# Optimization experiments

Measured on AMD Instinct MI355X. Metric: run time of the kernel, lower is better.

Reference implementation:

```python
import jax, jax.numpy as jnp
import numpy as np

PAIR = 128
HID = 64
EPS = 1e-5


def _ln(x, w, b):
    mu = jnp.mean(x, axis=-1, keepdims=True)
    var = jnp.mean((x - mu) ** 2, axis=-1, keepdims=True)
    return (x - mu) * jax.lax.rsqrt(var + EPS) * w + b


def setup_inputs() -> dict:
    key = jax.random.key(0)
    ks = jax.random.split(key, 8)
    B, N = 1, 448
    s_in = 1.0 / np.sqrt(PAIR)
    s_h = 1.0 / np.sqrt(HID)
    return {
        "z": jax.random.normal(ks[0], (B, N, N, PAIR), jnp.float32),
        "z_mask": jnp.ones((B, N, N), jnp.float32),
        "ln_w": jnp.ones((PAIR,), jnp.float32),
        "ln_b": jnp.zeros((PAIR,), jnp.float32),
        "lnh_w": jnp.ones((HID,), jnp.float32),
        "lnh_b": jnp.zeros((HID,), jnp.float32),
        "g1_w": jax.random.uniform(ks[1], (PAIR, HID), jnp.float32, -s_in, s_in),
        "g1_b": jnp.zeros((HID,), jnp.float32),
        "g2_w": jax.random.uniform(ks[2], (PAIR, HID), jnp.float32, -s_in, s_in),
        "g2_b": jnp.zeros((HID,), jnp.float32),
        "l1_w": jax.random.uniform(ks[3], (PAIR, HID), jnp.float32, -s_in, s_in),
        "l1_b": jnp.zeros((HID,), jnp.float32),
        "l2_w": jax.random.uniform(ks[4], (PAIR, HID), jnp.float32, -s_in, s_in),
        "l2_b": jnp.zeros((HID,), jnp.float32),
        "eg_w": jax.random.uniform(ks[5], (PAIR, PAIR), jnp.float32, -s_in, s_in),
        "eg_b": jnp.zeros((PAIR,), jnp.float32),
        "out_w": jax.random.uniform(ks[6], (HID, PAIR), jnp.float32, -s_h, s_h),
        "out_b": jnp.zeros((PAIR,), jnp.float32),
    }


def reference(z, z_mask, ln_w, ln_b, lnh_w, lnh_b, g1_w, g1_b, g2_w, g2_b,
              l1_w, l1_b, l2_w, l2_b, eg_w, eg_b, out_w, out_b):
    m = z_mask[..., None]                      # [B,N,N,1]
    zn = _ln(z, ln_w, ln_b)                    # [B,N,N,P]
    ab1 = jax.nn.sigmoid(zn @ g1_w + g1_b) * (zn @ l1_w + l1_b) * m  # [B,N,N,H]
    ab2 = jax.nn.sigmoid(zn @ g2_w + g2_b) * (zn @ l2_w + l2_b) * m  # [B,N,N,H]
    # outgoing + incoming triangle products, per channel c
    block = (jnp.einsum('bikc,bjkc->bijc', ab1, ab2)
             + jnp.einsum('bkic,bkjc->bijc', ab1, ab2))              # [B,N,N,H]
    out = jax.nn.sigmoid(zn @ eg_w + eg_b) * (_ln(block, lnh_w, lnh_b) @ out_w + out_b) * m
    return out
```

## Files before the change

kernel.cpp:

```cpp
#include <hip/hip_runtime.h>
#include <stdint.h>

#define N 448
#define NN (N*N)
#define P 128
#define H 64
#define PN 512
#define CH (PN*N)

typedef __attribute__((ext_vector_type(8))) short bf16x8;
typedef __attribute__((ext_vector_type(4))) float f32x4;
typedef __attribute__((ext_vector_type(16))) float f32x16;

__device__ __forceinline__ ushort f2bf(float f) {
    uint u = __builtin_bit_cast(uint, f);
    uint r = u + 0x7FFFu + ((u >> 16) & 1u);
    return (ushort)(r >> 16);
}
__device__ __forceinline__ float bf2f(ushort h) {
    uint u = ((uint)h) << 16;
    return __builtin_bit_cast(float, u);
}
__device__ __forceinline__ float sigmoidf(float x) {
    return 1.0f / (1.0f + __expf(-x));
}
__device__ __forceinline__ uint cvtpk(float lo, float hi) {
    uint r;
    asm("v_cvt_pk_bf16_f32 %0, %1, %2" : "=v"(r) : "v"(lo), "v"(hi));
    return r;
}

__global__ void k_prep(const float* __restrict__ g1w, const float* __restrict__ l1w,
                       const float* __restrict__ g2w, const float* __restrict__ l2w,
                       const float* __restrict__ egw,
                       ushort* __restrict__ wfrag) {
    int idx = blockIdx.x*256 + threadIdx.x;
    for (int e = idx; e < 24*4*64*8; e += gridDim.x*256) {
        int b  = e & 7;
        int l  = (e >> 3) & 63;
        int ks = (e >> 9) & 3;
        int ct = e >> 11;
        int k   = ks*32 + 8*(l>>4) + b;
        int col = ct*16 + (l & 15);
        float v;
        if (col < 64)       v = g1w[k*64 + col];
        else if (col < 128) v = l1w[k*64 + col - 64];
        else if (col < 192) v = g2w[k*64 + col - 128];
        else if (col < 256) v = l2w[k*64 + col - 192];
        else                v = egw[k*128 + col - 256];
        wfrag[e] = f2bf(v);
    }
}

__global__ __launch_bounds__(256) void k_proj(
    const float* __restrict__ z, const float* __restrict__ mask,
    const float* __restrict__ lnw, const float* __restrict__ lnb,
    const float* __restrict__ g1b, const float* __restrict__ l1b,
    const float* __restrict__ g2b, const float* __restrict__ l2b,
    const float* __restrict__ egb,
    const ushort* __restrict__ wfrag,
    ushort* __restrict__ abt, ushort* __restrict__ gsig)
{
    __shared__ ushort zn[64*128];
    const int t = threadIdx.x;
    const int w = t >> 6, l = t & 63;
    const int i = blockIdx.x / 7, j0 = (blockIdx.x % 7) * 64;

    {
        const int p = t >> 2;
        const int q = t & 3;
        const float* zp = z + (size_t)(i*N + j0 + p)*P + q*32;
        float4 v[8];
        #pragma unroll
        for (int x = 0; x < 8; ++x) v[x] = *(const float4*)(zp + x*4);
        float s = 0.f, sq = 0.f;
        #pragma unroll
        for (int x = 0; x < 8; ++x) {
            s  += v[x].x + v[x].y + v[x].z + v[x].w;
            sq += v[x].x*v[x].x + v[x].y*v[x].y + v[x].z*v[x].z + v[x].w*v[x].w;
        }
        s += __shfl_xor(s, 1);  sq += __shfl_xor(sq, 1);
        s += __shfl_xor(s, 2);  sq += __shfl_xor(sq, 2);
        float mu   = s * (1.0f/128.0f);
        float var  = sq * (1.0f/128.0f) - mu*mu;
        float rstd = rsqrtf(var + 1e-5f);
        #pragma unroll
        for (int cc = 0; cc < 4; ++cc) {
            int chunk = q*4 + cc;
            const float* lwp = lnw + chunk*8;
            const float* lbp = lnb + chunk*8;
            float4 lwa = *(const float4*)(lwp), lwb = *(const float4*)(lwp+4);
            float4 lba = *(const float4*)(lbp), lbb = *(const float4*)(lbp+4);
            float4 va = v[cc*2], vb = v[cc*2+1];
            float n0 = (va.x - mu)*rstd*lwa.x + lba.x;
            float n1 = (va.y - mu)*rstd*lwa.y + lba.y;
            float n2 = (va.z - mu)*rstd*lwa.z + lba.z;
            float n3 = (va.w - mu)*rstd*lwa.w + lba.w;
            float n4 = (vb.x - mu)*rstd*lwb.x + lbb.x;
            float n5 = (vb.y - mu)*rstd*lwb.y + lbb.y;
            float n6 = (vb.z - mu)*rstd*lwb.z + lbb.z;
            float n7 = (vb.w - mu)*rstd*lwb.w + lbb.w;
            uint4 pk;
            pk.x = cvtpk(n0, n1);
            pk.y = cvtpk(n2, n3);
            pk.z = cvtpk(n4, n5);
            pk.w = cvtpk(n6, n7);
            uint boff = (uint)p*256u + (((uint)(chunk ^ (p & 7)) & 15u) << 4);
            *(uint4*)((char*)zn + boff) = pk;
        }
    }
    __syncthreads();

    const int half = w & 1, pair = w >> 1;
    const uint lr = l & 15, lk = l >> 4;
    const float* mrow = mask + (size_t)i*N + j0;
    const float* gb = pair ? g2b : g1b;
    const float* lb = pair ? l2b : l1b;

    #pragma unroll 1
    for (int sub = 0; sub < 2; ++sub) {
        const int ctg = pair*8 + half*2 + sub;
        const int ctl = ctg + 4;
        f32x4 ag[4], al[4];
        #pragma unroll
        for (int mi = 0; mi < 4; ++mi) { ag[mi] = (f32x4){0,0,0,0}; al[mi] = (f32x4){0,0,0,0}; }

        #pragma unroll
        for (int ks = 0; ks < 4; ++ks) {
            bf16x8 bg  = *(const bf16x8*)(wfrag + ((size_t)(ctg*4 + ks)*64 + l)*8);
            bf16x8 blf = *(const bf16x8*)(wfrag + ((size_t)(ctl*4 + ks)*64 + l)*8);
            #pragma unroll
            for (int mi = 0; mi < 4; ++mi) {
                uint row = mi*16u + lr;
                uint chunk = (uint)(ks*4) + lk;
                bf16x8 af = *(const bf16x8*)((const char*)zn + row*256u + (((chunk ^ (row & 7u)) & 15u) << 4));
                ag[mi] = __builtin_amdgcn_mfma_f32_16x16x32_bf16(af, bg,  ag[mi], 0,0,0);
                al[mi] = __builtin_amdgcn_mfma_f32_16x16x32_bf16(af, blf, al[mi], 0,0,0);
            }
        }

        const int cidx = (half*2 + sub)*16 + (int)lr;
        const float gbias = gb[cidx];
        const float lbias = lb[cidx];
        #pragma unroll
        for (int mi = 0; mi < 4; ++mi) {
            float4 mv = *(const float4*)(mrow + mi*16 + (int)lk*4);
            float o0 = sigmoidf(ag[mi][0] + gbias) * (al[mi][0] + lbias) * mv.x;
            float o1 = sigmoidf(ag[mi][1] + gbias) * (al[mi][1] + lbias) * mv.y;
            float o2 = sigmoidf(ag[mi][2] + gbias) * (al[mi][2] + lbias) * mv.z;
            float o3 = sigmoidf(ag[mi][3] + gbias) * (al[mi][3] + lbias) * mv.w;
            uint2 pk;
            pk.x = cvtpk(o0, o1);
            pk.y = cvtpk(o2, o3);
            size_t off = (size_t)(pair*64 + cidx)*CH + (size_t)i*N + j0 + mi*16 + (int)lk*4;
            *(uint2*)(abt + off) = pk;
        }
    }

    {
        f32x4 ae[4][2];
        #pragma unroll
        for (int mi = 0; mi < 4; ++mi) { ae[mi][0] = (f32x4){0,0,0,0}; ae[mi][1] = (f32x4){0,0,0,0}; }

        #pragma unroll
        for (int ks = 0; ks < 4; ++ks) {
            bf16x8 b0 = *(const bf16x8*)(wfrag + ((size_t)((16 + w*2)*4 + ks)*64 + l)*8);
            bf16x8 b1 = *(const bf16x8*)(wfrag + ((size_t)((17 + w*2)*4 + ks)*64 + l)*8);
            #pragma unroll
            for (int mi = 0; mi < 4; ++mi) {
                uint row = mi*16u + lr;
                uint chunk = (uint)(ks*4) + lk;
                bf16x8 af = *(const bf16x8*)((const char*)zn + row*256u + (((chunk ^ (row & 7u)) & 15u) << 4));
                ae[mi][0] = __builtin_amdgcn_mfma_f32_16x16x32_bf16(af, b0, ae[mi][0], 0,0,0);
                ae[mi][1] = __builtin_amdgcn_mfma_f32_16x16x32_bf16(af, b1, ae[mi][1], 0,0,0);
            }
        }

        __syncthreads();

        float biasB[2];
        biasB[0] = egb[w*32 + (int)lr];
        biasB[1] = egb[w*32 + 16 + (int)lr];
        #pragma unroll
        for (int mi = 0; mi < 4; ++mi) {
            float4 mv = *(const float4*)(mrow + mi*16 + (int)lk*4);
            float mva[4] = { mv.x, mv.y, mv.z, mv.w };
            #pragma unroll
            for (int e = 0; e < 2; ++e) {
                uint cg = (uint)(w*32 + e*16) + lr;
                #pragma unroll
                for (int r = 0; r < 4; ++r) {
                    float sg = sigmoidf(ae[mi][e][r] + biasB[e]) * mva[r];
                    uint row = (uint)(mi*16) + lk*4u + (uint)r;
                    uint boff = row*256u + (((((cg >> 3) ^ (row & 7u)) & 15u)) << 4) + ((cg & 7u) << 1);
                    *(ushort*)((char*)zn + boff) = (ushort)cvtpk(sg, sg);
                }
            }
        }
    }
    __syncthreads();

    {
        int p2 = t >> 2, q2 = t & 3;
        size_t pos = (size_t)(i*N + j0 + p2);
        #pragma unroll
        for (int s2 = 0; s2 < 4; ++s2) {
            int chunk = q2*4 + s2;
            uint boff = (uint)p2*256u + (((uint)(chunk ^ (p2 & 7)) & 15u) << 4);
            uint4 vv = *(const uint4*)((const char*)zn + boff);
            *(uint4*)(gsig + pos*128 + q2*32 + s2*8) = vv;
        }
    }
}

__global__ __launch_bounds__(256) void k_transpose(const ushort* __restrict__ abt,
                                                   ushort* __restrict__ abtt) {
    int bid = blockIdx.x;
    int tile = bid % 49, a = bid / 49;
    int y0 = (tile / 7) * 64, x0 = (tile % 7) * 64;
    const ushort* src = abt  + (size_t)a*CH;
    ushort*       dst = abtt + (size_t)a*CH;
    __shared__ ushort tl[64][68];
    int t = threadIdx.x;
    #pragma unroll
    for (int q = 0; q < 4; ++q) {
        int f = q*1024 + t*4;
        int r = f >> 6, c4 = f & 63;
        ushort4 v = *(const ushort4*)(src + (size_t)(y0 + r)*N + x0 + c4);
        tl[r][c4] = v.x; tl[r][c4+1] = v.y; tl[r][c4+2] = v.z; tl[r][c4+3] = v.w;
    }
    __syncthreads();
    #pragma unroll
    for (int q = 0; q < 4; ++q) {
        int f = q*1024 + t*4;
        int r = f >> 6, c4 = f & 63;
        ushort4 v;
        v.x = tl[c4][r]; v.y = tl[c4+1][r]; v.z = tl[c4+2][r]; v.w = tl[c4+3][r];
        *(ushort4*)(dst + (size_t)(x0 + r)*N + y0 + c4) = v;
    }
}

__global__ __launch_bounds__(256) void k_tri(const ushort* __restrict__ abt,
                                             const ushort* __restrict__ abtt,
                                             float* __restrict__ blk) {
    int bid = (blockIdx.x & 7)*128 + (blockIdx.x >> 3);
    const int c = bid >> 4;
    const int tij = bid & 15;
    const int i0 = (tij >> 2) * 128, j0 = (tij & 3) * 128;
    const int t = threadIdx.x, w = t >> 6, l = t & 63;
    const int wr = w >> 1, wc = w & 1;
    const uint l31 = l & 31, kg = (uint)l >> 5;

    __shared__ ushort lds[4][128*64];

    const ushort* basep = (w >= 2) ? abtt : abt;
    const int chan = (w & 1) ? 64 + c : c;
    const int r0   = (w & 1) ? j0 : i0;
    const ushort* sbase = basep + (size_t)chan*CH + (size_t)r0*N;

    f32x16 acc[2][2];
    #pragma unroll
    for (int a = 0; a < 2; ++a)
        #pragma unroll
        for (int b = 0; b < 2; ++b) acc[a][b] = (f32x16){0,0,0,0,0,0,0,0,0,0,0,0,0,0,0,0};

    for (int kk = 0; kk < 7; ++kk) {
        __syncthreads();
        const ushort* sb = sbase + kk*64;
        #pragma unroll
        for (int q = 0; q < 16; ++q) {
            int r  = q*8 + (l >> 3);
            int ch = (l & 7) ^ (r & 7);
            const ushort* g = sb + (size_t)r*N + ch*8;
            __builtin_amdgcn_global_load_lds(
                (const __attribute__((address_space(1))) uint*)g,
                (__attribute__((address_space(3))) uint*)(&lds[w][q*512]),
                16, 0, 0);
        }
        __syncthreads();

        #pragma unroll
        for (int ks = 0; ks < 4; ++ks) {
            const uint chunk = (uint)(ks*2) + kg;
            {
                bf16x8 aA[2], bB[2];
                #pragma unroll
                for (int x = 0; x < 2; ++x) {
                    uint rowa = (uint)wr*64u + (uint)x*32u + l31;
                    uint rowb = (uint)wc*64u + (uint)x*32u + l31;
                    aA[x] = *(const bf16x8*)((const char*)lds[0] + rowa*128u + (((chunk ^ (rowa & 7u)) & 15u) << 4));
                    bB[x] = *(const bf16x8*)((const char*)lds[1] + rowb*128u + (((chunk ^ (rowb & 7u)) & 15u) << 4));
                }
                #pragma unroll
                for (int ra = 0; ra < 2; ++ra)
                    #pragma unroll
                    for (int cb = 0; cb < 2; ++cb)
                        acc[ra][cb] = __builtin_amdgcn_mfma_f32_32x32x16_bf16(aA[ra], bB[cb], acc[ra][cb], 0,0,0);
            }
            {
                bf16x8 aA[2], bB[2];
                #pragma unroll
                for (int x = 0; x < 2; ++x) {
                    uint rowa = (uint)wr*64u + (uint)x*32u + l31;
                    uint rowb = (uint)wc*64u + (uint)x*32u + l31;
                    aA[x] = *(const bf16x8*)((const char*)lds[2] + rowa*128u + (((chunk ^ (rowa & 7u)) & 15u) << 4));
                    bB[x] = *(const bf16x8*)((const char*)lds[3] + rowb*128u + (((chunk ^ (rowb & 7u)) & 15u) << 4));
                }
                #pragma unroll
                for (int ra = 0; ra < 2; ++ra)
                    #pragma unroll
                    for (int cb = 0; cb < 2; ++cb)
                        acc[ra][cb] = __builtin_amdgcn_mfma_f32_32x32x16_bf16(aA[ra], bB[cb], acc[ra][cb], 0,0,0);
            }
        }
    }

    #pragma unroll
    for (int ra = 0; ra < 2; ++ra) {
        #pragma unroll
        for (int cb = 0; cb < 2; ++cb) {
            int jb = j0 + wc*64 + cb*32 + (int)l31;
            if (jb < N) {
                #pragma unroll
                for (int r = 0; r < 16; ++r) {
                    int ii = i0 + wr*64 + ra*32 + (r & 3) + 8*(r >> 2) + 4*(int)kg;
                    if (ii < N) blk[(size_t)c*NN + (size_t)ii*N + jb] = acc[ra][cb][r];
                }
            }
        }
    }
}

__global__ __launch_bounds__(256) void k_out(const float* __restrict__ blk,
    const ushort* __restrict__ gsig,
    const float* __restrict__ lnhw, const float* __restrict__ lnhb,
    const float* __restrict__ outw, const float* __restrict__ outb,
    float* __restrict__ out)
{
    __shared__ float sblk[64][68];
    const int t = threadIdx.x;
    const int w = t >> 6, l = t & 63;
    const int pos0 = blockIdx.x * 64;

    #pragma unroll
    for (int q = 0; q < 4; ++q) {
        int flat = q*256 + t;
        int h = flat >> 4, f4 = flat & 15;
        float4 v = *(const float4*)(blk + (size_t)h*NN + pos0 + f4*4);
        sblk[f4*4+0][h] = v.x;
        sblk[f4*4+1][h] = v.y;
        sblk[f4*4+2][h] = v.z;
        sblk[f4*4+3][h] = v.w;
    }
    __syncthreads();

    {
        int p = w*16 + (l >> 2);
        int sub = l & 3;
        float vv[16];
        float s = 0.f, sq = 0.f;
        #pragma unroll
        for (int j = 0; j < 16; ++j) {
            float x = sblk[p][sub*16 + j];
            vv[j] = x; s += x; sq += x*x;
        }
        s += __shfl_xor(s, 1);  sq += __shfl_xor(sq, 1);
        s += __shfl_xor(s, 2);  sq += __shfl_xor(sq, 2);
        float mu   = s * (1.0f/64.0f);
        float var  = sq * (1.0f/64.0f) - mu*mu;
        float rstd = rsqrtf(var + 1e-5f);
        #pragma unroll
        for (int j = 0; j < 16; ++j) {
            float nv = (vv[j] - mu)*rstd*lnhw[sub*16+j] + lnhb[sub*16+j];
            sblk[p][sub*16 + j] = nv;
        }
    }
    __syncthreads();

    const int c4 = (t & 31) * 4;
    const int pg = t >> 5;
    float4 ob = *(const float4*)(outb + c4);

    #pragma unroll 1
    for (int hh = 0; hh < 2; ++hh) {
        const int prow = hh*32 + pg*4;
        float acc[4][4];
        #pragma unroll
        for (int j2 = 0; j2 < 4; ++j2)
            #pragma unroll
            for (int cc = 0; cc < 4; ++cc) acc[j2][cc] = 0.f;

        #pragma unroll 4
        for (int h4 = 0; h4 < 16; ++h4) {
            float4 wv[4];
            #pragma unroll
            for (int j = 0; j < 4; ++j)
                wv[j] = *(const float4*)(outw + (h4*4+j)*128 + c4);
            #pragma unroll
            for (int j2 = 0; j2 < 4; ++j2) {
                float4 av = *(const float4*)(&sblk[prow + j2][h4*4]);
                acc[j2][0] += av.x*wv[0].x + av.y*wv[1].x + av.z*wv[2].x + av.w*wv[3].x;
                acc[j2][1] += av.x*wv[0].y + av.y*wv[1].y + av.z*wv[2].y + av.w*wv[3].y;
                acc[j2][2] += av.x*wv[0].z + av.y*wv[1].z + av.z*wv[2].z + av.w*wv[3].z;
                acc[j2][3] += av.x*wv[0].w + av.y*wv[1].w + av.z*wv[2].w + av.w*wv[3].w;
            }
        }

        #pragma unroll
        for (int j2 = 0; j2 < 4; ++j2) {
            size_t pos = (size_t)(pos0 + prow + j2);
            ushort4 gv = *(const ushort4*)(gsig + pos*128 + c4);
            float4 res;
            res.x = bf2f(gv.x) * (acc[j2][0] + ob.x);
            res.y = bf2f(gv.y) * (acc[j2][1] + ob.y);
            res.z = bf2f(gv.z) * (acc[j2][2] + ob.z);
            res.w = bf2f(gv.w) * (acc[j2][3] + ob.w);
            *(float4*)(out + pos*128 + c4) = res;
        }
    }
}

extern "C" void kernel_launch(void* const* d_in, const int* in_sizes, int n_in,
                              void* d_out, int out_size, void* d_ws, size_t ws_size,
                              hipStream_t stream) {
    const float* z    = (const float*)d_in[0];
    const float* mask = (const float*)d_in[1];
    const float* lnw  = (const float*)d_in[2];
    const float* lnb  = (const float*)d_in[3];
    const float* lnhw = (const float*)d_in[4];
    const float* lnhb = (const float*)d_in[5];
    const float* g1w  = (const float*)d_in[6];
    const float* g1b  = (const float*)d_in[7];
    const float* g2w  = (const float*)d_in[8];
    const float* g2b  = (const float*)d_in[9];
    const float* l1w  = (const float*)d_in[10];
    const float* l1b  = (const float*)d_in[11];
    const float* l2w  = (const float*)d_in[12];
    const float* l2b  = (const float*)d_in[13];
    const float* egw  = (const float*)d_in[14];
    const float* egb  = (const float*)d_in[15];
    const float* outw = (const float*)d_in[16];
    const float* outb = (const float*)d_in[17];

    char* ws = (char*)d_ws;
    const size_t SZ_AB = (size_t)2*64*CH*2;
    const size_t SZ_G  = (size_t)NN*128*2;
    const size_t SZ_BL = (size_t)64*NN*4;
    ushort* abt    = (ushort*)ws;
    ushort* abtt   = (ushort*)(ws + SZ_AB);
    ushort* gsig   = (ushort*)(ws + 2*SZ_AB);
    float*  blkb   = (float*) (ws + 2*SZ_AB + SZ_G);
    ushort* wfrag  = (ushort*)(ws + 2*SZ_AB + SZ_G + SZ_BL);

    k_prep<<<32, 256, 0, stream>>>(g1w, l1w, g2w, l2w, egw, wfrag);
    k_proj<<<3136, 256, 0, stream>>>(z, mask, lnw, lnb, g1b, l1b, g2b, l2b, egb, wfrag, abt, gsig);
    k_transpose<<<128*49, 256, 0, stream>>>(abt, abtt);
    k_tri<<<64*16, 256, 0, stream>>>(abt, abtt, blkb);
    k_out<<<NN/64, 256, 0, stream>>>(blkb, gsig, lnhw, lnhb, outw, outb, (float*)d_out);
}
```

Baseline: 289.8 us.

## Split LayerNorm out of projection kernel and stage normalized z via direct LDS loads

The fused LayerNorm+projection kernel is split in two. A new kernel normalizes z and writes swizzled bf16 rows to a scratch buffer that reuses the block-output workspace. The matmul kernel then fills its LDS tile with global_load_lds direct-to-LDS copies. This is meant to shorten the matmul kernel's prologue and lower its register pressure, but it adds a launch and a bf16 round trip through global memory.

```diff
diff --git a/kernel.cpp b/kernel.cpp
--- a/kernel.cpp
+++ b/kernel.cpp
@@ -52,9 +52,57 @@
     }
 }
 
-__global__ __launch_bounds__(256) void k_proj(
-    const float* __restrict__ z, const float* __restrict__ mask,
+__global__ __launch_bounds__(256) void k_ln(
+    const float* __restrict__ z,
     const float* __restrict__ lnw, const float* __restrict__ lnb,
+    ushort* __restrict__ zng)
+{
+    const int t = threadIdx.x;
+    const int pos = blockIdx.x*64 + (t >> 2);
+    const int q = t & 3;
+    const float* zp = z + (size_t)pos*P + q*32;
+    float4 v[8];
+    #pragma unroll
+    for (int x = 0; x < 8; ++x) v[x] = *(const float4*)(zp + x*4);
+    float s = 0.f, sq = 0.f;
+    #pragma unroll
+    for (int x = 0; x < 8; ++x) {
+        s  += v[x].x + v[x].y + v[x].z + v[x].w;
+        sq += v[x].x*v[x].x + v[x].y*v[x].y + v[x].z*v[x].z + v[x].w*v[x].w;
+    }
+    s += __shfl_xor(s, 1);  sq += __shfl_xor(sq, 1);
+    s += __shfl_xor(s, 2);  sq += __shfl_xor(sq, 2);
+    float mu   = s * (1.0f/128.0f);
+    float var  = sq * (1.0f/128.0f) - mu*mu;
+    float rstd = rsqrtf(var + 1e-5f);
+    #pragma unroll
+    for (int cc = 0; cc < 4; ++cc) {
+        int chunk = q*4 + cc;
+        const float* lwp = lnw + chunk*8;
+        const float* lbp = lnb + chunk*8;
+        float4 lwa = *(const float4*)(lwp), lwb = *(const float4*)(lwp+4);
+        float4 lba = *(const float4*)(lbp), lbb = *(const float4*)(lbp+4);
+        float4 va = v[cc*2], vb = v[cc*2+1];
+        float n0 = (va.x - mu)*rstd*lwa.x + lba.x;
+        float n1 = (va.y - mu)*rstd*lwa.y + lba.y;
+        float n2 = (va.z - mu)*rstd*lwa.z + lba.z;
+        float n3 = (va.w - mu)*rstd*lwa.w + lba.w;
+        float n4 = (vb.x - mu)*rstd*lwb.x + lbb.x;
+        float n5 = (vb.y - mu)*rstd*lwb.y + lbb.y;
+        float n6 = (vb.z - mu)*rstd*lwb.z + lbb.z;
+        float n7 = (vb.w - mu)*rstd*lwb.w + lbb.w;
+        uint4 pk;
+        pk.x = cvtpk(n0, n1);
+        pk.y = cvtpk(n2, n3);
+        pk.z = cvtpk(n4, n5);
+        pk.w = cvtpk(n6, n7);
+        int slot = chunk ^ (pos & 7);
+        *(uint4*)(zng + (size_t)pos*128 + slot*8) = pk;
+    }
+}
+
+__global__ __launch_bounds__(256) void k_mm(
+    const ushort* __restrict__ zng, const float* __restrict__ mask,
     const float* __restrict__ g1b, const float* __restrict__ l1b,
     const float* __restrict__ g2b, const float* __restrict__ l2b,
     const float* __restrict__ egb,
@@ -67,46 +115,14 @@
     const int i = blockIdx.x / 7, j0 = (blockIdx.x % 7) * 64;
 
     {
-        const int p = t >> 2;
-        const int q = t & 3;
-        const float* zp = z + (size_t)(i*N + j0 + p)*P + q*32;
-        float4 v[8];
-        #pragma unroll
-        for (int x = 0; x < 8; ++x) v[x] = *(const float4*)(zp + x*4);
-        float s = 0.f, sq = 0.f;
-        #pragma unroll
-        for (int x = 0; x < 8; ++x) {
-            s  += v[x].x + v[x].y + v[x].z + v[x].w;
-            sq += v[x].x*v[x].x + v[x].y*v[x].y + v[x].z*v[x].z + v[x].w*v[x].w;
-        }
-        s += __shfl_xor(s, 1);  sq += __shfl_xor(sq, 1);
-        s += __shfl_xor(s, 2);  sq += __shfl_xor(sq, 2);
-        float mu   = s * (1.0f/128.0f);
-        float var  = sq * (1.0f/128.0f) - mu*mu;
-        float rstd = rsqrtf(var + 1e-5f);
-        #pragma unroll
-        for (int cc = 0; cc < 4; ++cc) {
-            int chunk = q*4 + cc;
-            const float* lwp = lnw + chunk*8;
-            const float* lbp = lnb + chunk*8;
-            float4 lwa = *(const float4*)(lwp), lwb = *(const float4*)(lwp+4);
-            float4 lba = *(const float4*)(lbp), lbb = *(const float4*)(lbp+4);
-            float4 va = v[cc*2], vb = v[cc*2+1];
-            float n0 = (va.x - mu)*rstd*lwa.x + lba.x;
-            float n1 = (va.y - mu)*rstd*lwa.y + lba.y;
-            float n2 = (va.z - mu)*rstd*lwa.z + lba.z;
-            float n3 = (va.w - mu)*rstd*lwa.w + lba.w;
-            float n4 = (vb.x - mu)*rstd*lwb.x + lbb.x;
-            float n5 = (vb.y - mu)*rstd*lwb.y + lbb.y;
-            float n6 = (vb.z - mu)*rstd*lwb.z + lbb.z;
-            float n7 = (vb.w - mu)*rstd*lwb.w + lbb.w;
-            uint4 pk;
-            pk.x = cvtpk(n0, n1);
-            pk.y = cvtpk(n2, n3);
-            pk.z = cvtpk(n4, n5);
-            pk.w = cvtpk(n6, n7);
-            uint boff = (uint)p*256u + (((uint)(chunk ^ (p & 7)) & 15u) << 4);
-            *(uint4*)((char*)zn + boff) = pk;
+        const ushort* src = zng + (size_t)(i*N + j0 + w*16)*128;
+        #pragma unroll
+        for (int qq = 0; qq < 4; ++qq) {
+            const ushort* g = src + (size_t)qq*512 + (l>>4)*128 + (l&15)*8;
+            __builtin_amdgcn_global_load_lds(
+                (const __attribute__((address_space(1))) uint*)g,
+                (__attribute__((address_space(3))) uint*)(&zn[(w*16 + qq*4)*128]),
+                16, 0, 0);
         }
     }
     __syncthreads();
@@ -451,9 +467,11 @@
     ushort* gsig   = (ushort*)(ws + 2*SZ_AB);
     float*  blkb   = (float*) (ws + 2*SZ_AB + SZ_G);
     ushort* wfrag  = (ushort*)(ws + 2*SZ_AB + SZ_G + SZ_BL);
+    ushort* zng    = (ushort*)blkb;
 
     k_prep<<<32, 256, 0, stream>>>(g1w, l1w, g2w, l2w, egw, wfrag);
-    k_proj<<<3136, 256, 0, stream>>>(z, mask, lnw, lnb, g1b, l1b, g2b, l2b, egb, wfrag, abt, gsig);
+    k_ln<<<3136, 256, 0, stream>>>(z, lnw, lnb, zng);
+    k_mm<<<3136, 256, 0, stream>>>(zng, mask, g1b, l1b, g2b, l2b, egb, wfrag, abt, gsig);
     k_transpose<<<128*49, 256, 0, stream>>>(abt, abtt);
     k_tri<<<64*16, 256, 0, stream>>>(abt, abtt, blkb);
     k_out<<<NN/64, 256, 0, stream>>>(blkb, gsig, lnhw, lnhb, outw, outb, (float*)d_out);
```

After: 307.0 us. 5.9% more time.

## Process two tiles per block in proj and out kernels with software pipelining

Applied to the files above, without the earlier changes.

k_proj now handles two i-rows per block. It prefetches the second row's z values into registers while the first row's matmuls run, and uses a double-buffered LDS with a separate gsig staging buffer. k_out handles four 64-position tiles per block, prefetching the next tile's block data into registers and alternating two LDS buffers. The aim is to hide global load latency behind compute. The cost is a quarter as many blocks in k_out, which lowers parallelism, plus more LDS and register use in both kernels, which may reduce occupancy.

```diff
diff --git a/kernel.cpp b/kernel.cpp
--- a/kernel.cpp
+++ b/kernel.cpp
@@ -52,71 +52,51 @@
     }
 }
 
-__global__ __launch_bounds__(256) void k_proj(
-    const float* __restrict__ z, const float* __restrict__ mask,
-    const float* __restrict__ lnw, const float* __restrict__ lnb,
-    const float* __restrict__ g1b, const float* __restrict__ l1b,
-    const float* __restrict__ g2b, const float* __restrict__ l2b,
-    const float* __restrict__ egb,
-    const ushort* __restrict__ wfrag,
-    ushort* __restrict__ abt, ushort* __restrict__ gsig)
-{
-    __shared__ ushort zn[64*128];
-    const int t = threadIdx.x;
-    const int w = t >> 6, l = t & 63;
-    const int i = blockIdx.x / 7, j0 = (blockIdx.x % 7) * 64;
-
-    {
-        const int p = t >> 2;
-        const int q = t & 3;
-        const float* zp = z + (size_t)(i*N + j0 + p)*P + q*32;
-        float4 v[8];
-        #pragma unroll
-        for (int x = 0; x < 8; ++x) v[x] = *(const float4*)(zp + x*4);
-        float s = 0.f, sq = 0.f;
-        #pragma unroll
-        for (int x = 0; x < 8; ++x) {
-            s  += v[x].x + v[x].y + v[x].z + v[x].w;
-            sq += v[x].x*v[x].x + v[x].y*v[x].y + v[x].z*v[x].z + v[x].w*v[x].w;
-        }
-        s += __shfl_xor(s, 1);  sq += __shfl_xor(sq, 1);
-        s += __shfl_xor(s, 2);  sq += __shfl_xor(sq, 2);
-        float mu   = s * (1.0f/128.0f);
-        float var  = sq * (1.0f/128.0f) - mu*mu;
-        float rstd = rsqrtf(var + 1e-5f);
-        #pragma unroll
-        for (int cc = 0; cc < 4; ++cc) {
-            int chunk = q*4 + cc;
-            const float* lwp = lnw + chunk*8;
-            const float* lbp = lnb + chunk*8;
-            float4 lwa = *(const float4*)(lwp), lwb = *(const float4*)(lwp+4);
-            float4 lba = *(const float4*)(lbp), lbb = *(const float4*)(lbp+4);
-            float4 va = v[cc*2], vb = v[cc*2+1];
-            float n0 = (va.x - mu)*rstd*lwa.x + lba.x;
-            float n1 = (va.y - mu)*rstd*lwa.y + lba.y;
-            float n2 = (va.z - mu)*rstd*lwa.z + lba.z;
-            float n3 = (va.w - mu)*rstd*lwa.w + lba.w;
-            float n4 = (vb.x - mu)*rstd*lwb.x + lbb.x;
-            float n5 = (vb.y - mu)*rstd*lwb.y + lbb.y;
-            float n6 = (vb.z - mu)*rstd*lwb.z + lbb.z;
-            float n7 = (vb.w - mu)*rstd*lwb.w + lbb.w;
-            uint4 pk;
-            pk.x = cvtpk(n0, n1);
-            pk.y = cvtpk(n2, n3);
-            pk.z = cvtpk(n4, n5);
-            pk.w = cvtpk(n6, n7);
-            uint boff = (uint)p*256u + (((uint)(chunk ^ (p & 7)) & 15u) << 4);
-            *(uint4*)((char*)zn + boff) = pk;
-        }
-    }
-    __syncthreads();
-
-    const int half = w & 1, pair = w >> 1;
+__device__ __forceinline__ void proj_ln(const float4* v, const float* __restrict__ lnw,
+                                        const float* __restrict__ lnb,
+                                        int p, int q, ushort* zn) {
+    float s = 0.f, sq = 0.f;
+    #pragma unroll
+    for (int x = 0; x < 8; ++x) {
+        s  += v[x].x + v[x].y + v[x].z + v[x].w;
+        sq += v[x].x*v[x].x + v[x].y*v[x].y + v[x].z*v[x].z + v[x].w*v[x].w;
+    }
+    s += __shfl_xor(s, 1);  sq += __shfl_xor(sq, 1);
+    s += __shfl_xor(s, 2);  sq += __shfl_xor(sq, 2);
+    float mu   = s * (1.0f/128.0f);
+    float var  = sq * (1.0f/128.0f) - mu*mu;
+    float rstd = rsqrtf(var + 1e-5f);
+    #pragma unroll
+    for (int cc = 0; cc < 4; ++cc) {
+        int chunk = q*4 + cc;
+        const float* lwp = lnw + chunk*8;
+        const float* lbp = lnb + chunk*8;
+        float4 lwa = *(const float4*)(lwp), lwb = *(const float4*)(lwp+4);
+        float4 lba = *(const float4*)(lbp), lbb = *(const float4*)(lbp+4);
+        float4 va = v[cc*2], vb = v[cc*2+1];
+        float n0 = (va.x - mu)*rstd*lwa.x + lba.x;
+        float n1 = (va.y - mu)*rstd*lwa.y + lba.y;
+        float n2 = (va.z - mu)*rstd*lwa.z + lba.z;
+        float n3 = (va.w - mu)*rstd*lwa.w + lba.w;
+        float n4 = (vb.x - mu)*rstd*lwb.x + lbb.x;
+        float n5 = (vb.y - mu)*rstd*lwb.y + lbb.y;
+        float n6 = (vb.z - mu)*rstd*lwb.z + lbb.z;
+        float n7 = (vb.w - mu)*rstd*lwb.w + lbb.w;
+        uint4 pk;
+        pk.x = cvtpk(n0, n1);
+        pk.y = cvtpk(n2, n3);
+        pk.z = cvtpk(n4, n5);
+        pk.w = cvtpk(n6, n7);
+        uint boff = (uint)p*256u + (((uint)(chunk ^ (p & 7)) & 15u) << 4);
+        *(uint4*)((char*)zn + boff) = pk;
+    }
+}
+
+__device__ __forceinline__ void proj_mm_ab(const ushort* zn, const ushort* __restrict__ wfrag,
+        const float* __restrict__ gb, const float* __restrict__ lb,
+        const float* __restrict__ mrow,
+        int i, int j0, int pair, int half, int l, ushort* __restrict__ abt) {
     const uint lr = l & 15, lk = l >> 4;
-    const float* mrow = mask + (size_t)i*N + j0;
-    const float* gb = pair ? g2b : g1b;
-    const float* lb = pair ? l2b : l1b;
-
     #pragma unroll 1
     for (int sub = 0; sub < 2; ++sub) {
         const int ctg = pair*8 + half*2 + sub;
@@ -124,7 +104,6 @@
         f32x4 ag[4], al[4];
         #pragma unroll
         for (int mi = 0; mi < 4; ++mi) { ag[mi] = (f32x4){0,0,0,0}; al[mi] = (f32x4){0,0,0,0}; }
-
         #pragma unroll
         for (int ks = 0; ks < 4; ++ks) {
             bf16x8 bg  = *(const bf16x8*)(wfrag + ((size_t)(ctg*4 + ks)*64 + l)*8);
@@ -138,7 +117,6 @@
                 al[mi] = __builtin_amdgcn_mfma_f32_16x16x32_bf16(af, blf, al[mi], 0,0,0);
             }
         }
-
         const int cidx = (half*2 + sub)*16 + (int)lr;
         const float gbias = gb[cidx];
         const float lbias = lb[cidx];
@@ -156,61 +134,113 @@
             *(uint2*)(abt + off) = pk;
         }
     }
-
+}
+
+__device__ __forceinline__ void proj_mm_eg(const ushort* zn, const ushort* __restrict__ wfrag,
+        const float* __restrict__ egb, const float* __restrict__ mrow,
+        int w, int l, ushort* gsbuf) {
+    const uint lr = l & 15, lk = l >> 4;
+    f32x4 ae[4][2];
+    #pragma unroll
+    for (int mi = 0; mi < 4; ++mi) { ae[mi][0] = (f32x4){0,0,0,0}; ae[mi][1] = (f32x4){0,0,0,0}; }
+    #pragma unroll
+    for (int ks = 0; ks < 4; ++ks) {
+        bf16x8 b0 = *(const bf16x8*)(wfrag + ((size_t)((16 + w*2)*4 + ks)*64 + l)*8);
+        bf16x8 b1 = *(const bf16x8*)(wfrag + ((size_t)((17 + w*2)*4 + ks)*64 + l)*8);
+        #pragma unroll
+        for (int mi = 0; mi < 4; ++mi) {
+            uint row = mi*16u + lr;
+            uint chunk = (uint)(ks*4) + lk;
+            bf16x8 af = *(const bf16x8*)((const char*)zn + row*256u + (((chunk ^ (row & 7u)) & 15u) << 4));
+            ae[mi][0] = __builtin_amdgcn_mfma_f32_16x16x32_bf16(af, b0, ae[mi][0], 0,0,0);
+            ae[mi][1] = __builtin_amdgcn_mfma_f32_16x16x32_bf16(af, b1, ae[mi][1], 0,0,0);
+        }
+    }
+    float biasB[2];
+    biasB[0] = egb[w*32 + (int)lr];
+    biasB[1] = egb[w*32 + 16 + (int)lr];
+    #pragma unroll
+    for (int mi = 0; mi < 4; ++mi) {
+        float4 mv = *(const float4*)(mrow + mi*16 + (int)lk*4);
+        float mva[4] = { mv.x, mv.y, mv.z, mv.w };
+        #pragma unroll
+        for (int e = 0; e < 2; ++e) {
+            uint cg = (uint)(w*32 + e*16) + lr;
+            #pragma unroll
+            for (int r = 0; r < 4; ++r) {
+                float sg = sigmoidf(ae[mi][e][r] + biasB[e]) * mva[r];
+                uint row = (uint)(mi*16) + lk*4u + (uint)r;
+                uint boff = row*256u + (((((cg >> 3) ^ (row & 7u)) & 15u)) << 4) + ((cg & 7u) << 1);
+                *(ushort*)((char*)gsbuf + boff) = (ushort)cvtpk(sg, sg);
+            }
+        }
+    }
+}
+
+__device__ __forceinline__ void proj_gsig_store(const ushort* gsbuf, ushort* __restrict__ gsig,
+        int i, int j0, int t) {
+    int p2 = t >> 2, q2 = t & 3;
+    size_t pos = (size_t)(i*N + j0 + p2);
+    #pragma unroll
+    for (int s2 = 0; s2 < 4; ++s2) {
+        int chunk = q2*4 + s2;
+        uint boff = (uint)p2*256u + (((uint)(chunk ^ (p2 & 7)) & 15u) << 4);
+        uint4 vv = *(const uint4*)((const char*)gsbuf + boff);
+        *(uint4*)(gsig + pos*128 + q2*32 + s2*8) = vv;
+    }
+}
+
+__global__ __launch_bounds__(256) void k_proj(
+    const float* __restrict__ z, const float* __restrict__ mask,
+    const float* __restrict__ lnw, const float* __restrict__ lnb,
+    const float* __restrict__ g1b, const float* __restrict__ l1b,
+    const float* __restrict__ g2b, const float* __restrict__ l2b,
+    const float* __restrict__ egb,
+    const ushort* __restrict__ wfrag,
+    ushort* __restrict__ abt, ushort* __restrict__ gsig)
+{
+    __shared__ ushort zn2[2][64*128];
+    __shared__ ushort gsbuf[64*128];
+    const int t = threadIdx.x;
+    const int w = t >> 6, l = t & 63;
+    const int ia = (blockIdx.x / 7) * 2, ib = ia + 1;
+    const int j0 = (blockIdx.x % 7) * 64;
+    const int p = t >> 2, q = t & 3;
+    const int half = w & 1, pair = w >> 1;
+    const float* mrowA = mask + (size_t)ia*N + j0;
+    const float* mrowB = mask + (size_t)ib*N + j0;
+    const float* gb = pair ? g2b : g1b;
+    const float* lb = pair ? l2b : l1b;
+
+    float4 vA[8];
     {
-        f32x4 ae[4][2];
-        #pragma unroll
-        for (int mi = 0; mi < 4; ++mi) { ae[mi][0] = (f32x4){0,0,0,0}; ae[mi][1] = (f32x4){0,0,0,0}; }
-
-        #pragma unroll
-        for (int ks = 0; ks < 4; ++ks) {
-            bf16x8 b0 = *(const bf16x8*)(wfrag + ((size_t)((16 + w*2)*4 + ks)*64 + l)*8);
-            bf16x8 b1 = *(const bf16x8*)(wfrag + ((size_t)((17 + w*2)*4 + ks)*64 + l)*8);
-            #pragma unroll
-            for (int mi = 0; mi < 4; ++mi) {
-                uint row = mi*16u + lr;
-                uint chunk = (uint)(ks*4) + lk;
-                bf16x8 af = *(const bf16x8*)((const char*)zn + row*256u + (((chunk ^ (row & 7u)) & 15u) << 4));
-                ae[mi][0] = __builtin_amdgcn_mfma_f32_16x16x32_bf16(af, b0, ae[mi][0], 0,0,0);
-                ae[mi][1] = __builtin_amdgcn_mfma_f32_16x16x32_bf16(af, b1, ae[mi][1], 0,0,0);
-            }
-        }
-
-        __syncthreads();
-
-        float biasB[2];
-        biasB[0] = egb[w*32 + (int)lr];
-        biasB[1] = egb[w*32 + 16 + (int)lr];
-        #pragma unroll
-        for (int mi = 0; mi < 4; ++mi) {
-            float4 mv = *(const float4*)(mrow + mi*16 + (int)lk*4);
-            float mva[4] = { mv.x, mv.y, mv.z, mv.w };
-            #pragma unroll
-            for (int e = 0; e < 2; ++e) {
-                uint cg = (uint)(w*32 + e*16) + lr;
-                #pragma unroll
-                for (int r = 0; r < 4; ++r) {
-                    float sg = sigmoidf(ae[mi][e][r] + biasB[e]) * mva[r];
-                    uint row = (uint)(mi*16) + lk*4u + (uint)r;
-                    uint boff = row*256u + (((((cg >> 3) ^ (row & 7u)) & 15u)) << 4) + ((cg & 7u) << 1);
-                    *(ushort*)((char*)zn + boff) = (ushort)cvtpk(sg, sg);
-                }
-            }
-        }
+        const float* zp = z + (size_t)(ia*N + j0 + p)*P + q*32;
+        #pragma unroll
+        for (int x = 0; x < 8; ++x) vA[x] = *(const float4*)(zp + x*4);
+    }
+    proj_ln(vA, lnw, lnb, p, q, zn2[0]);
+
+    float4 vB[8];
+    {
+        const float* zp = z + (size_t)(ib*N + j0 + p)*P + q*32;
+        #pragma unroll
+        for (int x = 0; x < 8; ++x) vB[x] = *(const float4*)(zp + x*4);
     }
     __syncthreads();
 
-    {
-        int p2 = t >> 2, q2 = t & 3;
-        size_t pos = (size_t)(i*N + j0 + p2);
-        #pragma unroll
-        for (int s2 = 0; s2 < 4; ++s2) {
-            int chunk = q2*4 + s2;
-            uint boff = (uint)p2*256u + (((uint)(chunk ^ (p2 & 7)) & 15u) << 4);
-            uint4 vv = *(const uint4*)((const char*)zn + boff);
-            *(uint4*)(gsig + pos*128 + q2*32 + s2*8) = vv;
-        }
-    }
+    proj_mm_ab(zn2[0], wfrag, gb, lb, mrowA, ia, j0, pair, half, l, abt);
+    proj_mm_eg(zn2[0], wfrag, egb, mrowA, w, l, gsbuf);
+    proj_ln(vB, lnw, lnb, p, q, zn2[1]);
+    __syncthreads();
+
+    proj_gsig_store(gsbuf, gsig, ia, j0, t);
+    proj_mm_ab(zn2[1], wfrag, gb, lb, mrowB, ib, j0, pair, half, l, abt);
+    __syncthreads();
+
+    proj_mm_eg(zn2[1], wfrag, egb, mrowB, w, l, gsbuf);
+    __syncthreads();
+
+    proj_gsig_store(gsbuf, gsig, ib, j0, t);
 }
 
 __global__ __launch_bounds__(256) void k_transpose(const ushort* __restrict__ abt,
@@ -337,85 +367,106 @@
     const float* __restrict__ outw, const float* __restrict__ outb,
     float* __restrict__ out)
 {
-    __shared__ float sblk[64][68];
+    __shared__ float sblk[2][64][68];
     const int t = threadIdx.x;
     const int w = t >> 6, l = t & 63;
-    const int pos0 = blockIdx.x * 64;
-
-    #pragma unroll
-    for (int q = 0; q < 4; ++q) {
-        int flat = q*256 + t;
+    const int base = blockIdx.x * 256;
+
+    float4 pre[4];
+    #pragma unroll
+    for (int qq = 0; qq < 4; ++qq) {
+        int flat = qq*256 + t;
         int h = flat >> 4, f4 = flat & 15;
-        float4 v = *(const float4*)(blk + (size_t)h*NN + pos0 + f4*4);
-        sblk[f4*4+0][h] = v.x;
-        sblk[f4*4+1][h] = v.y;
-        sblk[f4*4+2][h] = v.z;
-        sblk[f4*4+3][h] = v.w;
-    }
-    __syncthreads();
-
-    {
-        int p = w*16 + (l >> 2);
-        int sub = l & 3;
-        float vv[16];
-        float s = 0.f, sq = 0.f;
-        #pragma unroll
-        for (int j = 0; j < 16; ++j) {
-            float x = sblk[p][sub*16 + j];
-            vv[j] = x; s += x; sq += x*x;
-        }
-        s += __shfl_xor(s, 1);  sq += __shfl_xor(sq, 1);
-        s += __shfl_xor(s, 2);  sq += __shfl_xor(sq, 2);
-        float mu   = s * (1.0f/64.0f);
-        float var  = sq * (1.0f/64.0f) - mu*mu;
-        float rstd = rsqrtf(var + 1e-5f);
-        #pragma unroll
-        for (int j = 0; j < 16; ++j) {
-            float nv = (vv[j] - mu)*rstd*lnhw[sub*16+j] + lnhb[sub*16+j];
-            sblk[p][sub*16 + j] = nv;
-        }
-    }
-    __syncthreads();
-
-    const int c4 = (t & 31) * 4;
-    const int pg = t >> 5;
-    float4 ob = *(const float4*)(outb + c4);
+        pre[qq] = *(const float4*)(blk + (size_t)h*NN + base + f4*4);
+    }
 
     #pragma unroll 1
-    for (int hh = 0; hh < 2; ++hh) {
-        const int prow = hh*32 + pg*4;
-        float acc[4][4];
-        #pragma unroll
-        for (int j2 = 0; j2 < 4; ++j2)
-            #pragma unroll
-            for (int cc = 0; cc < 4; ++cc) acc[j2][cc] = 0.f;
-
-        #pragma unroll 4
-        for (int h4 = 0; h4 < 16; ++h4) {
-            float4 wv[4];
-            #pragma unroll
-            for (int j = 0; j < 4; ++j)
-                wv[j] = *(const float4*)(outw + (h4*4+j)*128 + c4);
+    for (int tt = 0; tt < 4; ++tt) {
+        const int b = tt & 1;
+        const int pos0 = base + tt*64;
+
+        #pragma unroll
+        for (int qq = 0; qq < 4; ++qq) {
+            int flat = qq*256 + t;
+            int h = flat >> 4, f4 = flat & 15;
+            sblk[b][f4*4+0][h] = pre[qq].x;
+            sblk[b][f4*4+1][h] = pre[qq].y;
+            sblk[b][f4*4+2][h] = pre[qq].z;
+            sblk[b][f4*4+3][h] = pre[qq].w;
+        }
+        if (tt < 3) {
+            #pragma unroll
+            for (int qq = 0; qq < 4; ++qq) {
+                int flat = qq*256 + t;
+                int h = flat >> 4, f4 = flat & 15;
+                pre[qq] = *(const float4*)(blk + (size_t)h*NN + pos0 + 64 + f4*4);
+            }
+        }
+        __syncthreads();
+
+        {
+            int p = w*16 + (l >> 2);
+            int sub = l & 3;
+            float vv[16];
+            float s = 0.f, sq = 0.f;
+            #pragma unroll
+            for (int j = 0; j < 16; ++j) {
+                float x = sblk[b][p][sub*16 + j];
+                vv[j] = x; s += x; sq += x*x;
+            }
+            s += __shfl_xor(s, 1);  sq += __shfl_xor(sq, 1);
+            s += __shfl_xor(s, 2);  sq += __shfl_xor(sq, 2);
+            float mu   = s * (1.0f/64.0f);
+            float var  = sq * (1.0f/64.0f) - mu*mu;
+            float rstd = rsqrtf(var + 1e-5f);
+            #pragma unroll
+            for (int j = 0; j < 16; ++j) {
+                float nv = (vv[j] - mu)*rstd*lnhw[sub*16+j] + lnhb[sub*16+j];
+                sblk[b][p][sub*16 + j] = nv;
+            }
+        }
+        __syncthreads();
+
+        const int c4 = (t & 31) * 4;
+        const int pg = t >> 5;
+        float4 ob = *(const float4*)(outb + c4);
+
+        #pragma unroll 1
+        for (int hh = 0; hh < 2; ++hh) {
+            const int prow = hh*32 + pg*4;
+            float acc[4][4];
+            #pragma unroll
+            for (int j2 = 0; j2 < 4; ++j2)
+                #pragma unroll
+                for (int cc = 0; cc < 4; ++cc) acc[j2][cc] = 0.f;
+
+            #pragma unroll 4
+            for (int h4 = 0; h4 < 16; ++h4) {
+                float4 wv[4];
+                #pragma unroll
+                for (int j = 0; j < 4; ++j)
+                    wv[j] = *(const float4*)(outw + (h4*4+j)*128 + c4);
+                #pragma unroll
+                for (int j2 = 0; j2 < 4; ++j2) {
+                    float4 av = *(const float4*)(&sblk[b][prow + j2][h4*4]);
+                    acc[j2][0] += av.x*wv[0].x + av.y*wv[1].x + av.z*wv[2].x + av.w*wv[3].x;
+                    acc[j2][1] += av.x*wv[0].y + av.y*wv[1].y + av.z*wv[2].y + av.w*wv[3].y;
+                    acc[j2][2] += av.x*wv[0].z + av.y*wv[1].z + av.z*wv[2].z + av.w*wv[3].z;
+                    acc[j2][3] += av.x*wv[0].w + av.y*wv[1].w + av.z*wv[2].w + av.w*wv[3].w;
+                }
+            }
+
             #pragma unroll
             for (int j2 = 0; j2 < 4; ++j2) {
-                float4 av = *(const float4*)(&sblk[prow + j2][h4*4]);
-                acc[j2][0] += av.x*wv[0].x + av.y*wv[1].x + av.z*wv[2].x + av.w*wv[3].x;
-                acc[j2][1] += av.x*wv[0].y + av.y*wv[1].y + av.z*wv[2].y + av.w*wv[3].y;
-                acc[j2][2] += av.x*wv[0].z + av.y*wv[1].z + av.z*wv[2].z + av.w*wv[3].z;
-                acc[j2][3] += av.x*wv[0].w + av.y*wv[1].w + av.z*wv[2].w + av.w*wv[3].w;
-            }
-        }
-
-        #pragma unroll
-        for (int j2 = 0; j2 < 4; ++j2) {
-            size_t pos = (size_t)(pos0 + prow + j2);
-            ushort4 gv = *(const ushort4*)(gsig + pos*128 + c4);
-            float4 res;
-            res.x = bf2f(gv.x) * (acc[j2][0] + ob.x);
-            res.y = bf2f(gv.y) * (acc[j2][1] + ob.y);
-            res.z = bf2f(gv.z) * (acc[j2][2] + ob.z);
-            res.w = bf2f(gv.w) * (acc[j2][3] + ob.w);
-            *(float4*)(out + pos*128 + c4) = res;
+                size_t pos = (size_t)(pos0 + prow + j2);
+                ushort4 gv = *(const ushort4*)(gsig + pos*128 + c4);
+                float4 res;
+                res.x = bf2f(gv.x) * (acc[j2][0] + ob.x);
+                res.y = bf2f(gv.y) * (acc[j2][1] + ob.y);
+                res.z = bf2f(gv.z) * (acc[j2][2] + ob.z);
+                res.w = bf2f(gv.w) * (acc[j2][3] + ob.w);
+                *(float4*)(out + pos*128 + c4) = res;
+            }
         }
     }
 }
@@ -453,8 +504,8 @@
     ushort* wfrag  = (ushort*)(ws + 2*SZ_AB + SZ_G + SZ_BL);
 
     k_prep<<<32, 256, 0, stream>>>(g1w, l1w, g2w, l2w, egw, wfrag);
-    k_proj<<<3136, 256, 0, stream>>>(z, mask, lnw, lnb, g1b, l1b, g2b, l2b, egb, wfrag, abt, gsig);
+    k_proj<<<1568, 256, 0, stream>>>(z, mask, lnw, lnb, g1b, l1b, g2b, l2b, egb, wfrag, abt, gsig);
     k_transpose<<<128*49, 256, 0, stream>>>(abt, abtt);
     k_tri<<<64*16, 256, 0, stream>>>(abt, abtt, blkb);
-    k_out<<<NN/64, 256, 0, stream>>>(blkb, gsig, lnhw, lnhb, outw, outb, (float*)d_out);
-}
+    k_out<<<NN/256, 256, 0, stream>>>(blkb, gsig, lnhw, lnhb, outw, outb, (float*)d_out);
+}
```

Measured after the change: 296.2 us. +2.2%, slower.

## Stage projection stores through LDS and prefetch blk tiles in output kernel

Applied to the files above, without the earlier changes.

In k_proj, the gated projection outputs are first written to a shared-memory staging tile and then copied to global memory as 16-byte coalesced rows, replacing scattered 8-byte stores. The mask loads are hoisted out of the loops and reused. k_out now processes four 64-position tiles per block, using a double-buffered LDS tile and prefetching the next tile's blk data into registers while the current one is normalised and projected. This adds shared memory per block, which may lower occupancy, and launches a quarter as many blocks for k_out.

```diff
diff --git a/kernel.cpp b/kernel.cpp
--- a/kernel.cpp
+++ b/kernel.cpp
@@ -62,6 +62,7 @@
     ushort* __restrict__ abt, ushort* __restrict__ gsig)
 {
     __shared__ ushort zn[64*128];
+    __shared__ ushort abstage[128*72];
     const int t = threadIdx.x;
     const int w = t >> 6, l = t & 63;
     const int i = blockIdx.x / 7, j0 = (blockIdx.x % 7) * 64;
@@ -117,6 +118,10 @@
     const float* gb = pair ? g2b : g1b;
     const float* lb = pair ? l2b : l1b;
 
+    float4 mv4[4];
+    #pragma unroll
+    for (int mi = 0; mi < 4; ++mi) mv4[mi] = *(const float4*)(mrow + mi*16 + (int)lk*4);
+
     #pragma unroll 1
     for (int sub = 0; sub < 2; ++sub) {
         const int ctg = pair*8 + half*2 + sub;
@@ -142,9 +147,10 @@
         const int cidx = (half*2 + sub)*16 + (int)lr;
         const float gbias = gb[cidx];
         const float lbias = lb[cidx];
+        const int srow = pair*64 + cidx;
         #pragma unroll
         for (int mi = 0; mi < 4; ++mi) {
-            float4 mv = *(const float4*)(mrow + mi*16 + (int)lk*4);
+            float4 mv = mv4[mi];
             float o0 = sigmoidf(ag[mi][0] + gbias) * (al[mi][0] + lbias) * mv.x;
             float o1 = sigmoidf(ag[mi][1] + gbias) * (al[mi][1] + lbias) * mv.y;
             float o2 = sigmoidf(ag[mi][2] + gbias) * (al[mi][2] + lbias) * mv.z;
@@ -152,8 +158,19 @@
             uint2 pk;
             pk.x = cvtpk(o0, o1);
             pk.y = cvtpk(o2, o3);
-            size_t off = (size_t)(pair*64 + cidx)*CH + (size_t)i*N + j0 + mi*16 + (int)lk*4;
-            *(uint2*)(abt + off) = pk;
+            *(uint2*)(abstage + (size_t)srow*72 + mi*16 + (int)lk*4) = pk;
+        }
+    }
+    __syncthreads();
+
+    {
+        int r = t >> 1, hh2 = t & 1;
+        const ushort* sp = abstage + (size_t)r*72 + hh2*32;
+        ushort* dp = abt + (size_t)r*CH + (size_t)i*N + j0 + hh2*32;
+        #pragma unroll
+        for (int k2 = 0; k2 < 4; ++k2) {
+            uint4 vv = *(const uint4*)(sp + k2*8);
+            *(uint4*)(dp + k2*8) = vv;
         }
     }
 
@@ -183,7 +200,7 @@
         biasB[1] = egb[w*32 + 16 + (int)lr];
         #pragma unroll
         for (int mi = 0; mi < 4; ++mi) {
-            float4 mv = *(const float4*)(mrow + mi*16 + (int)lk*4);
+            float4 mv = mv4[mi];
             float mva[4] = { mv.x, mv.y, mv.z, mv.w };
             #pragma unroll
             for (int e = 0; e < 2; ++e) {
@@ -337,85 +354,106 @@
     const float* __restrict__ outw, const float* __restrict__ outb,
     float* __restrict__ out)
 {
-    __shared__ float sblk[64][68];
+    __shared__ float sblk[2][64][68];
     const int t = threadIdx.x;
     const int w = t >> 6, l = t & 63;
-    const int pos0 = blockIdx.x * 64;
-
-    #pragma unroll
-    for (int q = 0; q < 4; ++q) {
-        int flat = q*256 + t;
+    const int base = blockIdx.x * 256;
+
+    float4 pre[4];
+    #pragma unroll
+    for (int qq = 0; qq < 4; ++qq) {
+        int flat = qq*256 + t;
         int h = flat >> 4, f4 = flat & 15;
-        float4 v = *(const float4*)(blk + (size_t)h*NN + pos0 + f4*4);
-        sblk[f4*4+0][h] = v.x;
-        sblk[f4*4+1][h] = v.y;
-        sblk[f4*4+2][h] = v.z;
-        sblk[f4*4+3][h] = v.w;
-    }
-    __syncthreads();
-
-    {
-        int p = w*16 + (l >> 2);
-        int sub = l & 3;
-        float vv[16];
-        float s = 0.f, sq = 0.f;
-        #pragma unroll
-        for (int j = 0; j < 16; ++j) {
-            float x = sblk[p][sub*16 + j];
-            vv[j] = x; s += x; sq += x*x;
-        }
-        s += __shfl_xor(s, 1);  sq += __shfl_xor(sq, 1);
-        s += __shfl_xor(s, 2);  sq += __shfl_xor(sq, 2);
-        float mu   = s * (1.0f/64.0f);
-        float var  = sq * (1.0f/64.0f) - mu*mu;
-        float rstd = rsqrtf(var + 1e-5f);
-        #pragma unroll
-        for (int j = 0; j < 16; ++j) {
-            float nv = (vv[j] - mu)*rstd*lnhw[sub*16+j] + lnhb[sub*16+j];
-            sblk[p][sub*16 + j] = nv;
-        }
-    }
-    __syncthreads();
-
-    const int c4 = (t & 31) * 4;
-    const int pg = t >> 5;
-    float4 ob = *(const float4*)(outb + c4);
+        pre[qq] = *(const float4*)(blk + (size_t)h*NN + base + f4*4);
+    }
 
     #pragma unroll 1
-    for (int hh = 0; hh < 2; ++hh) {
-        const int prow = hh*32 + pg*4;
-        float acc[4][4];
-        #pragma unroll
-        for (int j2 = 0; j2 < 4; ++j2)
-            #pragma unroll
-            for (int cc = 0; cc < 4; ++cc) acc[j2][cc] = 0.f;
-
-        #pragma unroll 4
-        for (int h4 = 0; h4 < 16; ++h4) {
-            float4 wv[4];
-            #pragma unroll
-            for (int j = 0; j < 4; ++j)
-                wv[j] = *(const float4*)(outw + (h4*4+j)*128 + c4);
+    for (int tt = 0; tt < 4; ++tt) {
+        const int b = tt & 1;
+        const int pos0 = base + tt*64;
+
+        #pragma unroll
+        for (int qq = 0; qq < 4; ++qq) {
+            int flat = qq*256 + t;
+            int h = flat >> 4, f4 = flat & 15;
+            sblk[b][f4*4+0][h] = pre[qq].x;
+            sblk[b][f4*4+1][h] = pre[qq].y;
+            sblk[b][f4*4+2][h] = pre[qq].z;
+            sblk[b][f4*4+3][h] = pre[qq].w;
+        }
+        if (tt < 3) {
+            #pragma unroll
+            for (int qq = 0; qq < 4; ++qq) {
+                int flat = qq*256 + t;
+                int h = flat >> 4, f4 = flat & 15;
+                pre[qq] = *(const float4*)(blk + (size_t)h*NN + pos0 + 64 + f4*4);
+            }
+        }
+        __syncthreads();
+
+        {
+            int p = w*16 + (l >> 2);
+            int sub = l & 3;
+            float vv[16];
+            float s = 0.f, sq = 0.f;
+            #pragma unroll
+            for (int j = 0; j < 16; ++j) {
+                float x = sblk[b][p][sub*16 + j];
+                vv[j] = x; s += x; sq += x*x;
+            }
+            s += __shfl_xor(s, 1);  sq += __shfl_xor(sq, 1);
+            s += __shfl_xor(s, 2);  sq += __shfl_xor(sq, 2);
+            float mu   = s * (1.0f/64.0f);
+            float var  = sq * (1.0f/64.0f) - mu*mu;
+            float rstd = rsqrtf(var + 1e-5f);
+            #pragma unroll
+            for (int j = 0; j < 16; ++j) {
+                float nv = (vv[j] - mu)*rstd*lnhw[sub*16+j] + lnhb[sub*16+j];
+                sblk[b][p][sub*16 + j] = nv;
+            }
+        }
+        __syncthreads();
+
+        const int c4 = (t & 31) * 4;
+        const int pg = t >> 5;
+        float4 ob = *(const float4*)(outb + c4);
+
+        #pragma unroll 1
+        for (int hh = 0; hh < 2; ++hh) {
+            const int prow = hh*32 + pg*4;
+            float acc[4][4];
+            #pragma unroll
+            for (int j2 = 0; j2 < 4; ++j2)
+                #pragma unroll
+                for (int cc = 0; cc < 4; ++cc) acc[j2][cc] = 0.f;
+
+            #pragma unroll 4
+            for (int h4 = 0; h4 < 16; ++h4) {
+                float4 wv[4];
+                #pragma unroll
+                for (int j = 0; j < 4; ++j)
+                    wv[j] = *(const float4*)(outw + (h4*4+j)*128 + c4);
+                #pragma unroll
+                for (int j2 = 0; j2 < 4; ++j2) {
+                    float4 av = *(const float4*)(&sblk[b][prow + j2][h4*4]);
+                    acc[j2][0] += av.x*wv[0].x + av.y*wv[1].x + av.z*wv[2].x + av.w*wv[3].x;
+                    acc[j2][1] += av.x*wv[0].y + av.y*wv[1].y + av.z*wv[2].y + av.w*wv[3].y;
+                    acc[j2][2] += av.x*wv[0].z + av.y*wv[1].z + av.z*wv[2].z + av.w*wv[3].z;
+                    acc[j2][3] += av.x*wv[0].w + av.y*wv[1].w + av.z*wv[2].w + av.w*wv[3].w;
+                }
+            }
+
             #pragma unroll
             for (int j2 = 0; j2 < 4; ++j2) {
-                float4 av = *(const float4*)(&sblk[prow + j2][h4*4]);
-                acc[j2][0] += av.x*wv[0].x + av.y*wv[1].x + av.z*wv[2].x + av.w*wv[3].x;
-                acc[j2][1] += av.x*wv[0].y + av.y*wv[1].y + av.z*wv[2].y + av.w*wv[3].y;
-                acc[j2][2] += av.x*wv[0].z + av.y*wv[1].z + av.z*wv[2].z + av.w*wv[3].z;
-                acc[j2][3] += av.x*wv[0].w + av.y*wv[1].w + av.z*wv[2].w + av.w*wv[3].w;
-            }
-        }
-
-        #pragma unroll
-        for (int j2 = 0; j2 < 4; ++j2) {
-            size_t pos = (size_t)(pos0 + prow + j2);
-            ushort4 gv = *(const ushort4*)(gsig + pos*128 + c4);
-            float4 res;
-            res.x = bf2f(gv.x) * (acc[j2][0] + ob.x);
-            res.y = bf2f(gv.y) * (acc[j2][1] + ob.y);
-            res.z = bf2f(gv.z) * (acc[j2][2] + ob.z);
-            res.w = bf2f(gv.w) * (acc[j2][3] + ob.w);
-            *(float4*)(out + pos*128 + c4) = res;
+                size_t pos = (size_t)(pos0 + prow + j2);
+                ushort4 gv = *(const ushort4*)(gsig + pos*128 + c4);
+                float4 res;
+                res.x = bf2f(gv.x) * (acc[j2][0] + ob.x);
+                res.y = bf2f(gv.y) * (acc[j2][1] + ob.y);
+                res.z = bf2f(gv.z) * (acc[j2][2] + ob.z);
+                res.w = bf2f(gv.w) * (acc[j2][3] + ob.w);
+                *(float4*)(out + pos*128 + c4) = res;
+            }
         }
     }
 }
@@ -456,5 +494,5 @@
     k_proj<<<3136, 256, 0, stream>>>(z, mask, lnw, lnb, g1b, l1b, g2b, l2b, egb, wfrag, abt, gsig);
     k_transpose<<<128*49, 256, 0, stream>>>(abt, abtt);
     k_tri<<<64*16, 256, 0, stream>>>(abt, abtt, blkb);
-    k_out<<<NN/64, 256, 0, stream>>>(blkb, gsig, lnhw, lnhb, outw, outb, (float*)d_out);
-}
+    k_out<<<NN/256, 256, 0, stream>>>(blkb, gsig, lnhw, lnhb, outw, outb, (float*)d_out);
+}
```

Measured after the change: 290.2 us. Within noise of the previous version (+0.1%).
